# Kernel tuning notes

Hardware: AMD Instinct MI355X
Metric: run time of the kernel (lower is better)

The kernel has to match this reference:

```python
import jax, jax.numpy as jnp
import numpy as np

K = 7      # unfold_size
P = 3      # unfold_size // 2
EPS = 1e-5 # batchnorm eps


def _conv1x1(x, w, b=None):
    # x: (B,C,H,W), w: (O,C)
    y = jnp.einsum('bchw,oc->bohw', x, w)
    if b is not None:
        y = y + b[None, :, None, None]
    return y


def _bn(x, g, b, m, v):
    # eval-mode batchnorm over channel axis 1
    inv = jax.lax.rsqrt(v + EPS)
    return (x - m[None, :, None, None]) * (g * inv)[None, :, None, None] + b[None, :, None, None]


def setup_inputs() -> dict:
    key = jax.random.key(0)
    ks = jax.random.split(key, 18)
    B, C, MID, H, W = 8, 256, 64, 64, 64
    rn = lambda k, s, sc=1.0: jax.random.normal(k, s, dtype=jnp.float32) * sc
    ru = lambda k, s: jax.random.uniform(k, s, dtype=jnp.float32)
    return {
        'x':     rn(ks[0], (B, C, H, W)),
        'w_red': rn(ks[1], (MID, C), 0.05),
        'w_c':   rn(ks[2], (3, MID, MID, 3, 3), 0.05),
        'b_c':   rn(ks[3], (3, MID), 0.05),
        'bn_g':  ru(ks[4], (3, MID)) * 0.5 + 0.75,
        'bn_b':  rn(ks[5], (3, MID), 0.05),
        'bn_m':  rn(ks[6], (3, MID), 0.05),
        'bn_v':  ru(ks[7], (3, MID)) + 0.5,
        'w_out': rn(ks[8], (C, MID), 0.05),
        'b_out': rn(ks[9], (C,), 0.05),
        'bno_g': ru(ks[10], (C,)) * 0.5 + 0.75,
        'bno_b': rn(ks[11], (C,), 0.05),
        'bno_m': rn(ks[12], (C,), 0.05),
        'bno_v': ru(ks[13], (C,)) + 0.5,
        'w_f1':  rn(ks[14], (C, C), 0.05),
        'b_f1':  rn(ks[15], (C,), 0.05),
        'w_f2':  rn(ks[16], (C, C), 0.05),
        'b_f2':  rn(ks[17], (C,), 0.05),
    }


def reference(x, w_red, w_c, b_c, bn_g, bn_b, bn_m, bn_v,
              w_out, b_out, bno_g, bno_b, bno_m, bno_v,
              w_f1, b_f1, w_f2, b_f2):
    B, C, H, W = x.shape
    MID = w_red.shape[0]

    # channel reduction + L2 normalize over channels (F.normalize, eps=1e-12)
    q = _conv1x1(x, w_red)                                   # (B,MID,H,W)
    q = q / jnp.maximum(jnp.linalg.norm(q, axis=1, keepdims=True), 1e-12)

    # SelfCorrelationComputation: unfold KxK with padding P, multiply by center, clamp >= 0
    qp = jnp.pad(q, ((0, 0), (0, 0), (P, P), (P, P)))
    pats = jnp.stack([qp[:, :, i:i + H, j:j + W]
                      for i in range(K) for j in range(K)], axis=2)  # (B,MID,K*K,H,W)
    ss = jnp.maximum(pats * q[:, :, None], 0.0)              # (B,MID,49,H,W)

    # SelfSimilarityEncoder: conv3d with (1,ksize,ksize) kernel == batched 2D conv over (u,v)
    ss = ss.transpose(0, 3, 4, 1, 2).reshape(B * H * W, MID, K, K)  # (B*HW,MID,K,K)
    dn = ('NCHW', 'OIHW', 'NCHW')
    y = ss
    for i in range(3):  # unfold_size // 2 blocks; 7 -> 5 -> 3 -> 1
        y = jax.lax.conv_general_dilated(y, w_c[i], (1, 1), 'VALID', dimension_numbers=dn)
        y = y + b_c[i][None, :, None, None]
        y = jnp.maximum(_bn(y, bn_g[i], bn_b[i], bn_m[i], bn_v[i]), 0.0)
    y = y.mean(axis=(-1, -2)).reshape(B, H, W, MID).transpose(0, 3, 1, 2)  # (B,MID,H,W)
    feat = _bn(_conv1x1(y, w_out, b_out), bno_g, bno_b, bno_m, bno_v)      # (B,C,H,W)

    # residual + FFN (1x1 conv -> relu -> 1x1 conv)
    out = x + feat
    out = _conv1x1(jnp.maximum(_conv1x1(out, w_f1, b_f1), 0.0), w_f2, b_f2)
    return out
```

## Files before the change

kernel.cpp:

```cpp
#include <hip/hip_runtime.h>
#include <stdint.h>


typedef __attribute__((ext_vector_type(8))) __bf16 bf16x8;
typedef __attribute__((ext_vector_type(4))) float f32x4;

__device__ __forceinline__ ushort f2bf(float f) {
  uint32_t u = __builtin_bit_cast(uint32_t, f);
  u += 0x7fffu + ((u >> 16) & 1u);
  return (ushort)(u >> 16);
}
__device__ __forceinline__ float bfu(ushort h) {
  return __builtin_bit_cast(float, ((uint32_t)h) << 16);
}
__device__ __forceinline__ f32x4 mfma16(bf16x8 a, bf16x8 b, f32x4 c) {
  return __builtin_amdgcn_mfma_f32_16x16x32_bf16(a, b, c, 0, 0, 0);
}

union BV8 { uint4 v; ushort u[8]; };

#define OFF_WRT 0u
#define OFF_WCB 65536u
#define OFF_SHC 286720u
#define OFF_WOB 287488u
#define OFF_SHO 320256u
#define OFF_WF1 321280u
#define OFF_WF2 452352u
#define OFF_QN  583424u
#define OFF_Y   4777728u

__global__ __launch_bounds__(256) void k_prep(
    const float* __restrict__ w_red, const float* __restrict__ w_c, const float* __restrict__ b_c,
    const float* __restrict__ bn_g, const float* __restrict__ bn_b, const float* __restrict__ bn_m,
    const float* __restrict__ bn_v, const float* __restrict__ w_out, const float* __restrict__ b_out,
    const float* __restrict__ bno_g, const float* __restrict__ bno_b, const float* __restrict__ bno_m,
    const float* __restrict__ bno_v, const float* __restrict__ w_f1, const float* __restrict__ w_f2,
    float* __restrict__ w_red_t, ushort* __restrict__ wc_b, float* __restrict__ shift_c,
    ushort* __restrict__ w_out_b, float* __restrict__ shift_o,
    ushort* __restrict__ w_f1_b, ushort* __restrict__ w_f2_b)
{
  int i = blockIdx.x * 256 + threadIdx.x;
  if (i < 16384) {
    int c = i >> 6, m = i & 63;
    w_red_t[i] = w_red[m * 256 + c];
    return;
  }
  i -= 16384;
  if (i < 110592) {
    int c = i & 63, o = (i >> 6) & 63, st = i >> 12;
    int tap = st % 9, s = st / 9;
    float sc = bn_g[s * 64 + o] * rsqrtf(bn_v[s * 64 + o] + 1e-5f);
    wc_b[i] = f2bf(w_c[((s * 64 + o) * 64 + c) * 9 + tap] * sc);
    return;
  }
  i -= 110592;
  if (i < 192) {
    int s = i >> 6, o = i & 63;
    float sc = bn_g[s * 64 + o] * rsqrtf(bn_v[s * 64 + o] + 1e-5f);
    shift_c[i] = (b_c[i] - bn_m[i]) * sc + bn_b[i];
    return;
  }
  i -= 192;
  if (i < 16384) {
    int o = i >> 6;
    float sc = bno_g[o] * rsqrtf(bno_v[o] + 1e-5f);
    w_out_b[i] = f2bf(w_out[i] * sc);
    return;
  }
  i -= 16384;
  if (i < 256) {
    float sc = bno_g[i] * rsqrtf(bno_v[i] + 1e-5f);
    shift_o[i] = (b_out[i] - bno_m[i]) * sc + bno_b[i];
    return;
  }
  i -= 256;
  if (i < 65536) { w_f1_b[i] = f2bf(w_f1[i]); return; }
  i -= 65536;
  if (i < 65536) { w_f2_b[i] = f2bf(w_f2[i]); return; }
}

__global__ __launch_bounds__(256) void k_qnorm(
    const float* __restrict__ x, const float* __restrict__ w_red_t, ushort* __restrict__ qn)
{
  __shared__ float xs[64 * 64];
  __shared__ float wls[64 * 64];
  __shared__ float part[64 * 16];
  __shared__ float sinv[64];

  const int tid = threadIdx.x;
  const int pix0 = blockIdx.x * 64;
  const int b = pix0 >> 12;
  const int hw0 = pix0 & 4095;
  const int pxq = tid & 15, mq = tid >> 4;
  const int lr = tid >> 2, lseg = tid & 3;

  float acc[4][4] = {};

  for (int c0 = 0; c0 < 256; c0 += 64) {
    const float4* xg = (const float4*)(x + (size_t)(b * 256 + c0 + lr) * 4096 + hw0 + lseg * 16);
    float4* xd = (float4*)(xs + lr * 64 + lseg * 16);
    const float4* wg = (const float4*)(w_red_t + (c0 + lr) * 64 + lseg * 16);
    float4* wd = (float4*)(wls + lr * 64 + lseg * 16);
#pragma unroll
    for (int j = 0; j < 4; ++j) xd[j] = xg[j];
#pragma unroll
    for (int j = 0; j < 4; ++j) wd[j] = wg[j];
    __syncthreads();
    for (int c = 0; c < 64; ++c) {
      float4 xv = *(const float4*)(xs + c * 64 + pxq * 4);
      float4 wv = *(const float4*)(wls + c * 64 + mq * 4);
      float xa[4] = {xv.x, xv.y, xv.z, xv.w};
      float wa[4] = {wv.x, wv.y, wv.z, wv.w};
#pragma unroll
      for (int mi = 0; mi < 4; ++mi)
#pragma unroll
        for (int pi = 0; pi < 4; ++pi)
          acc[mi][pi] = fmaf(wa[mi], xa[pi], acc[mi][pi]);
    }
    __syncthreads();
  }

#pragma unroll
  for (int pi = 0; pi < 4; ++pi) {
    float s = 0.f;
#pragma unroll
    for (int mi = 0; mi < 4; ++mi) s += acc[mi][pi] * acc[mi][pi];
    part[(pxq * 4 + pi) * 16 + mq] = s;
  }
  __syncthreads();
  if (tid < 64) {
    float s = 0.f;
#pragma unroll
    for (int k = 0; k < 16; ++k) s += part[tid * 16 + k];
    sinv[tid] = 1.0f / fmaxf(sqrtf(s), 1e-12f);
  }
  __syncthreads();
#pragma unroll
  for (int pi = 0; pi < 4; ++pi) {
    const int px = pxq * 4 + pi;
    const float inv = sinv[px];
    ushort4 v;
    v.x = f2bf(acc[0][pi] * inv);
    v.y = f2bf(acc[1][pi] * inv);
    v.z = f2bf(acc[2][pi] * inv);
    v.w = f2bf(acc[3][pi] * inv);
    *(ushort4*)(qn + (size_t)(pix0 + px) * 64 + mq * 4) = v;
  }
}

#define SS_BYTES (49 * 16 * 64 * 2)
#define O1_BYTES (25 * 16 * 64 * 2)
#define SMEM_ENC (SS_BYTES + O1_BYTES)

__device__ __forceinline__ void load_af(bf16x8* af, const ushort* wbase, int o0, int n, int q) {
#pragma unroll
  for (int tap = 0; tap < 9; ++tap)
#pragma unroll
    for (int kc = 0; kc < 2; ++kc)
      af[tap * 2 + kc] = *(const bf16x8*)(wbase + (tap * 64 + o0 + n) * 64 + kc * 32 + q * 8);
}

__device__ __forceinline__ void store_act(ushort* buf, int pos, int n, int q, int o0,
                                          f32x4 acc, float4 sh) {
  ushort4 v;
  v.x = f2bf(fmaxf(acc[0] + sh.x, 0.0f));
  v.y = f2bf(fmaxf(acc[1] + sh.y, 0.0f));
  v.z = f2bf(fmaxf(acc[2] + sh.z, 0.0f));
  v.w = f2bf(fmaxf(acc[3] + sh.w, 0.0f));
  const int chunk = (o0 >> 3) + (q >> 1);
  *(ushort4*)(buf + (pos * 16 + n) * 64 + ((chunk ^ (n & 7)) * 8) + (q & 1) * 4) = v;
}

__global__ __launch_bounds__(512, 1) void k_encoder(
    const ushort* __restrict__ qn, const ushort* __restrict__ wc_b,
    const float* __restrict__ shift_c, ushort* __restrict__ yout)
{
  extern __shared__ char smem[];
  ushort* ss = (ushort*)smem;
  ushort* o1 = (ushort*)(smem + SS_BYTES);
  ushort* o2 = (ushort*)smem;

  const int tid = threadIdx.x;
  const int b = blockIdx.z;
  const int tr = blockIdx.y * 4;
  const int tc = blockIdx.x * 4;

  {
    const int p = tid & 15;
    const int g = tid >> 4;
    const int ph = tr + (p >> 2), pw = tc + (p & 3);
    const ushort* cen = qn + (size_t)((b << 12) + ph * 64 + pw) * 64;
    const int swp = p & 7;
#pragma unroll
    for (int ch = 0; ch < 8; ++ch) {
      BV8 cv; cv.v = *(const uint4*)(cen + ch * 8);
      float cf[8];
#pragma unroll
      for (int j = 0; j < 8; ++j) cf[j] = bfu(cv.u[j]);
      for (int uv = g; uv < 49; uv += 32) {
        const int du = uv / 7 - 3, dv = uv % 7 - 3;
        const int nh = ph + du, nw = pw + dv;
        BV8 ov;
        if ((unsigned)nh < 64u && (unsigned)nw < 64u) {
          BV8 nv; nv.v = *(const uint4*)(qn + (size_t)((b << 12) + nh * 64 + nw) * 64 + ch * 8);
#pragma unroll
          for (int j = 0; j < 8; ++j)
            ov.u[j] = f2bf(fmaxf(bfu(nv.u[j]) * cf[j], 0.0f));
        } else {
          ov.v = make_uint4(0u, 0u, 0u, 0u);
        }
        *(uint4*)(ss + (uv * 16 + p) * 64 + ((ch ^ swp) * 8)) = ov.v;
      }
    }
  }
  __syncthreads();

  const int lane = tid & 63, wv = tid >> 6;
  const int n = lane & 15, q = lane >> 4;
  const int o0 = (wv & 3) * 16;
  const int h = wv >> 2;
  const int sw = n & 7;
  const int rowoff = n * 64;
  const int c0 = ((0 + q) ^ sw) * 8;
  const int c1 = ((4 + q) ^ sw) * 8;

  bf16x8 af[18];
  const f32x4 zero = {0.f, 0.f, 0.f, 0.f};

  load_af(af, wc_b, o0, n, q);
  {
    const float4 sh = *(const float4*)(shift_c + o0 + q * 4);
    const int ubeg = h ? 3 : 0, uend = h ? 5 : 3;
    for (int u = ubeg; u < uend; ++u) {
      f32x4 acc[5][2];
#pragma unroll
      for (int v = 0; v < 5; ++v) { acc[v][0] = zero; acc[v][1] = zero; }
#pragma unroll
      for (int du = 0; du < 3; ++du) {
        const ushort* rowb = ss + (u + du) * 7 * 1024 + rowoff;
        bf16x8 rf0[7], rf1[7];
#pragma unroll
        for (int j = 0; j < 7; ++j) {
          rf0[j] = *(const bf16x8*)(rowb + j * 1024 + c0);
          rf1[j] = *(const bf16x8*)(rowb + j * 1024 + c1);
        }
#pragma unroll
        for (int dv = 0; dv < 3; ++dv) {
#pragma unroll
          for (int v = 0; v < 5; ++v) {
            acc[v][0] = mfma16(af[(du * 3 + dv) * 2],     rf0[v + dv], acc[v][0]);
            acc[v][1] = mfma16(af[(du * 3 + dv) * 2 + 1], rf1[v + dv], acc[v][1]);
          }
        }
      }
#pragma unroll
      for (int v = 0; v < 5; ++v)
        store_act(o1, u * 5 + v, n, q, o0, acc[v][0] + acc[v][1], sh);
    }
  }
  __syncthreads();

  load_af(af, wc_b + 9 * 4096, o0, n, q);
  {
    const float4 sh = *(const float4*)(shift_c + 64 + o0 + q * 4);
    const int ubeg = h ? 2 : 0, uend = h ? 3 : 2;
    for (int u = ubeg; u < uend; ++u) {
      f32x4 acc[3][2];
#pragma unroll
      for (int v = 0; v < 3; ++v) { acc[v][0] = zero; acc[v][1] = zero; }
#pragma unroll
      for (int du = 0; du < 3; ++du) {
        const ushort* rowb = o1 + (u + du) * 5 * 1024 + rowoff;
        bf16x8 rf0[5], rf1[5];
#pragma unroll
        for (int j = 0; j < 5; ++j) {
          rf0[j] = *(const bf16x8*)(rowb + j * 1024 + c0);
          rf1[j] = *(const bf16x8*)(rowb + j * 1024 + c1);
        }
#pragma unroll
        for (int dv = 0; dv < 3; ++dv) {
#pragma unroll
          for (int v = 0; v < 3; ++v) {
            acc[v][0] = mfma16(af[(du * 3 + dv) * 2],     rf0[v + dv], acc[v][0]);
            acc[v][1] = mfma16(af[(du * 3 + dv) * 2 + 1], rf1[v + dv], acc[v][1]);
          }
        }
      }
#pragma unroll
      for (int v = 0; v < 3; ++v)
        store_act(o2, u * 3 + v, n, q, o0, acc[v][0] + acc[v][1], sh);
    }
  }
  __syncthreads();

  if (h == 0) {
    load_af(af, wc_b + 18 * 4096, o0, n, q);
    const float4 sh = *(const float4*)(shift_c + 128 + o0 + q * 4);
    f32x4 a0 = zero, a1 = zero;
#pragma unroll
    for (int tap = 0; tap < 9; ++tap) {
      const ushort* rA = o2 + tap * 1024 + rowoff;
      a0 = mfma16(af[tap * 2],     *(const bf16x8*)(rA + c0), a0);
      a1 = mfma16(af[tap * 2 + 1], *(const bf16x8*)(rA + c1), a1);
    }
    f32x4 acc = a0 + a1;
    ushort4 v;
    v.x = f2bf(fmaxf(acc[0] + sh.x, 0.0f));
    v.y = f2bf(fmaxf(acc[1] + sh.y, 0.0f));
    v.z = f2bf(fmaxf(acc[2] + sh.z, 0.0f));
    v.w = f2bf(fmaxf(acc[3] + sh.w, 0.0f));
    const int ph = tr + (n >> 2), pw = tc + (n & 3);
    *(ushort4*)(yout + (size_t)((b << 12) + ph * 64 + pw) * 64 + o0 + q * 4) = v;
  }
}

#define SMEM_OUT (2 * 64 * 256 * 2)

__global__ __launch_bounds__(256) void k_out(
    const ushort* __restrict__ y, const float* __restrict__ x,
    const ushort* __restrict__ w_out_b, const float* __restrict__ shift_o,
    const ushort* __restrict__ w_f1_b, const float* __restrict__ b_f1,
    const ushort* __restrict__ w_f2_b, const float* __restrict__ b_f2,
    float* __restrict__ out)
{
  extern __shared__ char smem[];
  ushort* rls = (ushort*)smem;
  ushort* hls = (ushort*)(smem + 64 * 256 * 2);

  const int tid = threadIdx.x, lane = tid & 63, wv = tid >> 6;
  const int n = lane & 15, q = lane >> 4;
  const int pix0 = blockIdx.x * 64;
  const int b = pix0 >> 12, hw0 = pix0 & 4095;
  const int sw = n & 7;
  const f32x4 zero = {0.f, 0.f, 0.f, 0.f};

  {
    bf16x8 wa[8];
#pragma unroll
    for (int mt = 0; mt < 4; ++mt) {
      const int ob = wv * 64 + mt * 16;
      wa[mt * 2]     = *(const bf16x8*)(w_out_b + (ob + n) * 64 + q * 8);
      wa[mt * 2 + 1] = *(const bf16x8*)(w_out_b + (ob + n) * 64 + 32 + q * 8);
    }
    for (int nt = 0; nt < 4; ++nt) {
      const int px0 = nt * 16;
      const bf16x8 yb0 = *(const bf16x8*)(y + (size_t)(pix0 + px0 + n) * 64 + q * 8);
      const bf16x8 yb1 = *(const bf16x8*)(y + (size_t)(pix0 + px0 + n) * 64 + 32 + q * 8);
#pragma unroll
      for (int mt = 0; mt < 4; ++mt) {
        const int ob = wv * 64 + mt * 16;
        f32x4 acc = zero;
        acc = mfma16(wa[mt * 2], yb0, acc);
        acc = mfma16(wa[mt * 2 + 1], yb1, acc);
        const float4 sh = *(const float4*)(shift_o + ob + q * 4);
        const float sha[4] = {sh.x, sh.y, sh.z, sh.w};
        ushort tmp[4];
#pragma unroll
        for (int r = 0; r < 4; ++r) {
          const int o = ob + q * 4 + r;
          const float xv = x[(size_t)(b * 256 + o) * 4096 + hw0 + px0 + n];
          tmp[r] = f2bf(xv + acc[r] + sha[r]);
        }
        ushort4 v; v.x = tmp[0]; v.y = tmp[1]; v.z = tmp[2]; v.w = tmp[3];
        const int chunk = (ob >> 3) + (q >> 1);
        *(ushort4*)(rls + (px0 + n) * 256 + ((chunk ^ sw) * 8) + (q & 1) * 4) = v;
      }
    }
  }
  __syncthreads();

  {
    bf16x8 wf[32];
#pragma unroll
    for (int mt = 0; mt < 4; ++mt)
#pragma unroll
      for (int kc = 0; kc < 8; ++kc)
        wf[mt * 8 + kc] = *(const bf16x8*)(w_f1_b + (size_t)(wv * 64 + mt * 16 + n) * 256 + kc * 32 + q * 8);
    for (int nt = 0; nt < 4; ++nt) {
      const int px0 = nt * 16;
      bf16x8 rb[8];
#pragma unroll
      for (int kc = 0; kc < 8; ++kc)
        rb[kc] = *(const bf16x8*)(rls + (px0 + n) * 256 + (((kc * 4 + q) ^ sw) * 8));
#pragma unroll
      for (int mt = 0; mt < 4; ++mt) {
        const int ob = wv * 64 + mt * 16;
        f32x4 a0 = zero, a1 = zero;
#pragma unroll
        for (int kc = 0; kc < 8; kc += 2) {
          a0 = mfma16(wf[mt * 8 + kc], rb[kc], a0);
          a1 = mfma16(wf[mt * 8 + kc + 1], rb[kc + 1], a1);
        }
        f32x4 acc = a0 + a1;
        const float4 bb = *(const float4*)(b_f1 + ob + q * 4);
        const float bba[4] = {bb.x, bb.y, bb.z, bb.w};
        ushort tmp[4];
#pragma unroll
        for (int r = 0; r < 4; ++r) tmp[r] = f2bf(fmaxf(acc[r] + bba[r], 0.0f));
        ushort4 v; v.x = tmp[0]; v.y = tmp[1]; v.z = tmp[2]; v.w = tmp[3];
        const int chunk = (ob >> 3) + (q >> 1);
        *(ushort4*)(hls + (px0 + n) * 256 + ((chunk ^ sw) * 8) + (q & 1) * 4) = v;
      }
    }
  }
  __syncthreads();

  {
    bf16x8 wf[32];
#pragma unroll
    for (int mt = 0; mt < 4; ++mt)
#pragma unroll
      for (int kc = 0; kc < 8; ++kc)
        wf[mt * 8 + kc] = *(const bf16x8*)(w_f2_b + (size_t)(wv * 64 + mt * 16 + n) * 256 + kc * 32 + q * 8);
    for (int nt = 0; nt < 4; ++nt) {
      const int px0 = nt * 16;
      bf16x8 rb[8];
#pragma unroll
      for (int kc = 0; kc < 8; ++kc)
        rb[kc] = *(const bf16x8*)(hls + (px0 + n) * 256 + (((kc * 4 + q) ^ sw) * 8));
#pragma unroll
      for (int mt = 0; mt < 4; ++mt) {
        const int ob = wv * 64 + mt * 16;
        f32x4 a0 = zero, a1 = zero;
#pragma unroll
        for (int kc = 0; kc < 8; kc += 2) {
          a0 = mfma16(wf[mt * 8 + kc], rb[kc], a0);
          a1 = mfma16(wf[mt * 8 + kc + 1], rb[kc + 1], a1);
        }
        f32x4 acc = a0 + a1;
        const float4 bb = *(const float4*)(b_f2 + ob + q * 4);
        const float bba[4] = {bb.x, bb.y, bb.z, bb.w};
#pragma unroll
        for (int r = 0; r < 4; ++r) {
          const int o = ob + q * 4 + r;
          out[(size_t)(b * 256 + o) * 4096 + hw0 + px0 + n] = acc[r] + bba[r];
        }
      }
    }
  }
}

extern "C" void kernel_launch(void* const* d_in, const int* in_sizes, int n_in,
                              void* d_out, int out_size, void* d_ws, size_t ws_size,
                              hipStream_t stream) {
  const float* x     = (const float*)d_in[0];
  const float* w_red = (const float*)d_in[1];
  const float* w_c   = (const float*)d_in[2];
  const float* b_c   = (const float*)d_in[3];
  const float* bn_g  = (const float*)d_in[4];
  const float* bn_b  = (const float*)d_in[5];
  const float* bn_m  = (const float*)d_in[6];
  const float* bn_v  = (const float*)d_in[7];
  const float* w_out = (const float*)d_in[8];
  const float* b_out = (const float*)d_in[9];
  const float* bno_g = (const float*)d_in[10];
  const float* bno_b = (const float*)d_in[11];
  const float* bno_m = (const float*)d_in[12];
  const float* bno_v = (const float*)d_in[13];
  const float* w_f1  = (const float*)d_in[14];
  const float* b_f1  = (const float*)d_in[15];
  const float* w_f2  = (const float*)d_in[16];
  const float* b_f2  = (const float*)d_in[17];

  char* ws = (char*)d_ws;
  float*  w_red_t = (float*)(ws + OFF_WRT);
  ushort* wc_b    = (ushort*)(ws + OFF_WCB);
  float*  shift_c = (float*)(ws + OFF_SHC);
  ushort* w_out_b = (ushort*)(ws + OFF_WOB);
  float*  shift_o = (float*)(ws + OFF_SHO);
  ushort* w_f1_b  = (ushort*)(ws + OFF_WF1);
  ushort* w_f2_b  = (ushort*)(ws + OFF_WF2);
  ushort* qnb     = (ushort*)(ws + OFF_QN);
  ushort* yb      = (ushort*)(ws + OFF_Y);

  k_prep<<<1074, 256, 0, stream>>>(w_red, w_c, b_c, bn_g, bn_b, bn_m, bn_v,
                                   w_out, b_out, bno_g, bno_b, bno_m, bno_v,
                                   w_f1, w_f2,
                                   w_red_t, wc_b, shift_c, w_out_b, shift_o, w_f1_b, w_f2_b);
  k_qnorm<<<512, 256, 0, stream>>>(x, w_red_t, qnb);
  k_encoder<<<dim3(16, 16, 8), 512, SMEM_ENC, stream>>>(qnb, wc_b, shift_c, yb);
  k_out<<<512, 256, SMEM_OUT, stream>>>(yb, x, w_out_b, shift_o, w_f1_b, b_f1, w_f2_b, b_f2,
                                        (float*)d_out);
}
```

Measured before the change: 323.7 us.

## Double encoder block to 1024 threads with templated 4-way conv work split

The encoder block now launches 1024 threads (16 waves) instead of 512. Each conv stage's output positions are split four ways across wave groups through a templated conv_block, and the K dimension is walked in two sequential halves so each wave holds only 9 weight fragments instead of 18. The self-similarity build gives each thread one fixed neighbor offset instead of a strided loop. The aim is more waves for latency hiding and lower register pressure, at the cost of an unbalanced split in the last stage and reloading weights per half.

```diff
diff --git a/kernel.cpp b/kernel.cpp
--- a/kernel.cpp
+++ b/kernel.cpp
@@ -152,14 +152,6 @@
 #define O1_BYTES (25 * 16 * 64 * 2)
 #define SMEM_ENC (SS_BYTES + O1_BYTES)
 
-__device__ __forceinline__ void load_af(bf16x8* af, const ushort* wbase, int o0, int n, int q) {
-#pragma unroll
-  for (int tap = 0; tap < 9; ++tap)
-#pragma unroll
-    for (int kc = 0; kc < 2; ++kc)
-      af[tap * 2 + kc] = *(const bf16x8*)(wbase + (tap * 64 + o0 + n) * 64 + kc * 32 + q * 8);
-}
-
 __device__ __forceinline__ void store_act(ushort* buf, int pos, int n, int q, int o0,
                                           f32x4 acc, float4 sh) {
   ushort4 v;
@@ -171,7 +163,53 @@
   *(ushort4*)(buf + (pos * 16 + n) * 64 + ((chunk ^ (n & 7)) * 8) + (q & 1) * 4) = v;
 }
 
-__global__ __launch_bounds__(512, 1) void k_encoder(
+template<int RS, int DS, int UB, int UE, int VB, int VE>
+__device__ __forceinline__ void conv_block(
+    const ushort* __restrict__ src, ushort* dst,
+    const ushort* __restrict__ wbase, const float* __restrict__ shiftp,
+    int n, int q, int o0, int rowoff, int c0, int c1)
+{
+  constexpr int NU = UE - UB, NV = VE - VB, NR = VE + 2 - VB;
+  const f32x4 zero = {0.f, 0.f, 0.f, 0.f};
+  f32x4 acc[NU][NV];
+#pragma unroll
+  for (int a = 0; a < NU; ++a)
+#pragma unroll
+    for (int bb = 0; bb < NV; ++bb) acc[a][bb] = zero;
+
+#pragma unroll 1
+  for (int kc = 0; kc < 2; ++kc) {
+    const int cc = kc ? c1 : c0;
+    bf16x8 af[9];
+#pragma unroll
+    for (int t = 0; t < 9; ++t)
+      af[t] = *(const bf16x8*)(wbase + (t * 64 + o0 + n) * 64 + kc * 32 + q * 8);
+#pragma unroll
+    for (int u = UB; u < UE; ++u) {
+#pragma unroll
+      for (int du = 0; du < 3; ++du) {
+        const ushort* rowb = src + (u + du) * RS * 1024 + rowoff;
+        bf16x8 rf[NR];
+#pragma unroll
+        for (int j = 0; j < NR; ++j)
+          rf[j] = *(const bf16x8*)(rowb + (VB + j) * 1024 + cc);
+#pragma unroll
+        for (int dv = 0; dv < 3; ++dv)
+#pragma unroll
+          for (int v = 0; v < NV; ++v)
+            acc[u - UB][v] = mfma16(af[du * 3 + dv], rf[v + dv], acc[u - UB][v]);
+      }
+    }
+  }
+  const float4 sh = *(const float4*)(shiftp + o0 + q * 4);
+#pragma unroll
+  for (int u = UB; u < UE; ++u)
+#pragma unroll
+    for (int v = 0; v < NV; ++v)
+      store_act(dst, u * DS + VB + v, n, q, o0, acc[u - UB][v], sh);
+}
+
+__global__ __launch_bounds__(1024) void k_encoder(
     const ushort* __restrict__ qn, const ushort* __restrict__ wc_b,
     const float* __restrict__ shift_c, ushort* __restrict__ yout)
 {
@@ -188,28 +226,29 @@
   {
     const int p = tid & 15;
     const int g = tid >> 4;
-    const int ph = tr + (p >> 2), pw = tc + (p & 3);
-    const ushort* cen = qn + (size_t)((b << 12) + ph * 64 + pw) * 64;
-    const int swp = p & 7;
-#pragma unroll
-    for (int ch = 0; ch < 8; ++ch) {
-      BV8 cv; cv.v = *(const uint4*)(cen + ch * 8);
-      float cf[8];
-#pragma unroll
-      for (int j = 0; j < 8; ++j) cf[j] = bfu(cv.u[j]);
-      for (int uv = g; uv < 49; uv += 32) {
-        const int du = uv / 7 - 3, dv = uv % 7 - 3;
-        const int nh = ph + du, nw = pw + dv;
-        BV8 ov;
-        if ((unsigned)nh < 64u && (unsigned)nw < 64u) {
-          BV8 nv; nv.v = *(const uint4*)(qn + (size_t)((b << 12) + nh * 64 + nw) * 64 + ch * 8);
+    if (g < 49) {
+      const int ph = tr + (p >> 2), pw = tc + (p & 3);
+      const ushort* cen = qn + (size_t)((b << 12) + ph * 64 + pw) * 64;
+      const int swp = p & 7;
+      const int du = g / 7 - 3, dv = g % 7 - 3;
+      const int nh = ph + du, nw = pw + dv;
+      if ((unsigned)nh < 64u && (unsigned)nw < 64u) {
+        const ushort* nb = qn + (size_t)((b << 12) + nh * 64 + nw) * 64;
+#pragma unroll
+        for (int ch = 0; ch < 8; ++ch) {
+          BV8 cv; cv.v = *(const uint4*)(cen + ch * 8);
+          BV8 nv; nv.v = *(const uint4*)(nb + ch * 8);
+          BV8 ov;
 #pragma unroll
           for (int j = 0; j < 8; ++j)
-            ov.u[j] = f2bf(fmaxf(bfu(nv.u[j]) * cf[j], 0.0f));
-        } else {
-          ov.v = make_uint4(0u, 0u, 0u, 0u);
+            ov.u[j] = f2bf(fmaxf(bfu(nv.u[j]) * bfu(cv.u[j]), 0.0f));
+          *(uint4*)(ss + (g * 16 + p) * 64 + ((ch ^ swp) * 8)) = ov.v;
         }
-        *(uint4*)(ss + (uv * 16 + p) * 64 + ((ch ^ swp) * 8)) = ov.v;
+      } else {
+        const uint4 z = make_uint4(0u, 0u, 0u, 0u);
+#pragma unroll
+        for (int ch = 0; ch < 8; ++ch)
+          *(uint4*)(ss + (g * 16 + p) * 64 + ((ch ^ swp) * 8)) = z;
       }
     }
   }
@@ -218,92 +257,54 @@
   const int lane = tid & 63, wv = tid >> 6;
   const int n = lane & 15, q = lane >> 4;
   const int o0 = (wv & 3) * 16;
-  const int h = wv >> 2;
+  const int G = wv >> 2;
   const int sw = n & 7;
   const int rowoff = n * 64;
   const int c0 = ((0 + q) ^ sw) * 8;
   const int c1 = ((4 + q) ^ sw) * 8;
 
-  bf16x8 af[18];
-  const f32x4 zero = {0.f, 0.f, 0.f, 0.f};
-
-  load_af(af, wc_b, o0, n, q);
-  {
-    const float4 sh = *(const float4*)(shift_c + o0 + q * 4);
-    const int ubeg = h ? 3 : 0, uend = h ? 5 : 3;
-    for (int u = ubeg; u < uend; ++u) {
-      f32x4 acc[5][2];
-#pragma unroll
-      for (int v = 0; v < 5; ++v) { acc[v][0] = zero; acc[v][1] = zero; }
-#pragma unroll
-      for (int du = 0; du < 3; ++du) {
-        const ushort* rowb = ss + (u + du) * 7 * 1024 + rowoff;
-        bf16x8 rf0[7], rf1[7];
-#pragma unroll
-        for (int j = 0; j < 7; ++j) {
-          rf0[j] = *(const bf16x8*)(rowb + j * 1024 + c0);
-          rf1[j] = *(const bf16x8*)(rowb + j * 1024 + c1);
-        }
-#pragma unroll
-        for (int dv = 0; dv < 3; ++dv) {
-#pragma unroll
-          for (int v = 0; v < 5; ++v) {
-            acc[v][0] = mfma16(af[(du * 3 + dv) * 2],     rf0[v + dv], acc[v][0]);
-            acc[v][1] = mfma16(af[(du * 3 + dv) * 2 + 1], rf1[v + dv], acc[v][1]);
-          }
-        }
-      }
-#pragma unroll
-      for (int v = 0; v < 5; ++v)
-        store_act(o1, u * 5 + v, n, q, o0, acc[v][0] + acc[v][1], sh);
-    }
-  }
-  __syncthreads();
-
-  load_af(af, wc_b + 9 * 4096, o0, n, q);
-  {
-    const float4 sh = *(const float4*)(shift_c + 64 + o0 + q * 4);
-    const int ubeg = h ? 2 : 0, uend = h ? 3 : 2;
-    for (int u = ubeg; u < uend; ++u) {
-      f32x4 acc[3][2];
-#pragma unroll
-      for (int v = 0; v < 3; ++v) { acc[v][0] = zero; acc[v][1] = zero; }
-#pragma unroll
-      for (int du = 0; du < 3; ++du) {
-        const ushort* rowb = o1 + (u + du) * 5 * 1024 + rowoff;
-        bf16x8 rf0[5], rf1[5];
-#pragma unroll
-        for (int j = 0; j < 5; ++j) {
-          rf0[j] = *(const bf16x8*)(rowb + j * 1024 + c0);
-          rf1[j] = *(const bf16x8*)(rowb + j * 1024 + c1);
-        }
-#pragma unroll
-        for (int dv = 0; dv < 3; ++dv) {
-#pragma unroll
-          for (int v = 0; v < 3; ++v) {
-            acc[v][0] = mfma16(af[(du * 3 + dv) * 2],     rf0[v + dv], acc[v][0]);
-            acc[v][1] = mfma16(af[(du * 3 + dv) * 2 + 1], rf1[v + dv], acc[v][1]);
-          }
-        }
-      }
-#pragma unroll
-      for (int v = 0; v < 3; ++v)
-        store_act(o2, u * 3 + v, n, q, o0, acc[v][0] + acc[v][1], sh);
-    }
-  }
-  __syncthreads();
-
-  if (h == 0) {
-    load_af(af, wc_b + 18 * 4096, o0, n, q);
+  {
+    const ushort* w1 = wc_b;
+    if (G == 0)
+      conv_block<7, 5, 0, 2, 0, 5>(ss, o1, w1, shift_c, n, q, o0, rowoff, c0, c1);
+    else if (G == 1)
+      conv_block<7, 5, 2, 4, 0, 5>(ss, o1, w1, shift_c, n, q, o0, rowoff, c0, c1);
+    else if (G == 2)
+      conv_block<7, 5, 4, 5, 0, 3>(ss, o1, w1, shift_c, n, q, o0, rowoff, c0, c1);
+    else
+      conv_block<7, 5, 4, 5, 3, 5>(ss, o1, w1, shift_c, n, q, o0, rowoff, c0, c1);
+  }
+  __syncthreads();
+
+  {
+    const ushort* w2 = wc_b + 9 * 4096;
+    const float* sh2 = shift_c + 64;
+    if (G == 0)
+      conv_block<5, 3, 0, 1, 0, 3>(o1, o2, w2, sh2, n, q, o0, rowoff, c0, c1);
+    else if (G == 1)
+      conv_block<5, 3, 1, 2, 0, 3>(o1, o2, w2, sh2, n, q, o0, rowoff, c0, c1);
+    else if (G == 2)
+      conv_block<5, 3, 2, 3, 0, 2>(o1, o2, w2, sh2, n, q, o0, rowoff, c0, c1);
+    else
+      conv_block<5, 3, 2, 3, 2, 3>(o1, o2, w2, sh2, n, q, o0, rowoff, c0, c1);
+  }
+  __syncthreads();
+
+  if (G == 0) {
+    const ushort* w3 = wc_b + 18 * 4096;
+    const f32x4 zero = {0.f, 0.f, 0.f, 0.f};
+    f32x4 acc = zero;
+#pragma unroll 1
+    for (int kc = 0; kc < 2; ++kc) {
+      const int cc = kc ? c1 : c0;
+#pragma unroll
+      for (int t = 0; t < 9; ++t) {
+        bf16x8 a = *(const bf16x8*)(w3 + (t * 64 + o0 + n) * 64 + kc * 32 + q * 8);
+        bf16x8 r = *(const bf16x8*)(o2 + t * 1024 + rowoff + cc);
+        acc = mfma16(a, r, acc);
+      }
+    }
     const float4 sh = *(const float4*)(shift_c + 128 + o0 + q * 4);
-    f32x4 a0 = zero, a1 = zero;
-#pragma unroll
-    for (int tap = 0; tap < 9; ++tap) {
-      const ushort* rA = o2 + tap * 1024 + rowoff;
-      a0 = mfma16(af[tap * 2],     *(const bf16x8*)(rA + c0), a0);
-      a1 = mfma16(af[tap * 2 + 1], *(const bf16x8*)(rA + c1), a1);
-    }
-    f32x4 acc = a0 + a1;
     ushort4 v;
     v.x = f2bf(fmaxf(acc[0] + sh.x, 0.0f));
     v.y = f2bf(fmaxf(acc[1] + sh.y, 0.0f));
@@ -478,7 +479,7 @@
                                    w_f1, w_f2,
                                    w_red_t, wc_b, shift_c, w_out_b, shift_o, w_f1_b, w_f2_b);
   k_qnorm<<<512, 256, 0, stream>>>(x, w_red_t, qnb);
-  k_encoder<<<dim3(16, 16, 8), 512, SMEM_ENC, stream>>>(qnb, wc_b, shift_c, yb);
+  k_encoder<<<dim3(16, 16, 8), 1024, SMEM_ENC, stream>>>(qnb, wc_b, shift_c, yb);
   k_out<<<512, 256, SMEM_OUT, stream>>>(yb, x, w_out_b, shift_o, w_f1_b, b_f1, w_f2_b, b_f2,
                                         (float*)d_out);
 }
```

Measured after the change: 366.8 us. 13.3% more time.

## Restructure encoder convs to load each input row once and raise occupancy

Applied to the files above, without the earlier changes.

Replaces the per-output-row conv loops with a templated conv2d_block that walks input rows once and accumulates into all output rows that use each row, cutting redundant LDS reads of shared rows. Each output position now uses a single accumulator chain instead of two split halves. Launch bounds are changed to allow two blocks per CU. The aim is fewer LDS loads and more latency hiding, at the cost of more live accumulator registers, which may cause spills or keep occupancy from rising given the large shared memory footprint.

```diff
diff --git a/kernel.cpp b/kernel.cpp
--- a/kernel.cpp
+++ b/kernel.cpp
@@ -152,14 +152,6 @@
 #define O1_BYTES (25 * 16 * 64 * 2)
 #define SMEM_ENC (SS_BYTES + O1_BYTES)
 
-__device__ __forceinline__ void load_af(bf16x8* af, const ushort* wbase, int o0, int n, int q) {
-#pragma unroll
-  for (int tap = 0; tap < 9; ++tap)
-#pragma unroll
-    for (int kc = 0; kc < 2; ++kc)
-      af[tap * 2 + kc] = *(const bf16x8*)(wbase + (tap * 64 + o0 + n) * 64 + kc * 32 + q * 8);
-}
-
 __device__ __forceinline__ void store_act(ushort* buf, int pos, int n, int q, int o0,
                                           f32x4 acc, float4 sh) {
   ushort4 v;
@@ -171,7 +163,59 @@
   *(ushort4*)(buf + (pos * 16 + n) * 64 + ((chunk ^ (n & 7)) * 8) + (q & 1) * 4) = v;
 }
 
-__global__ __launch_bounds__(512, 1) void k_encoder(
+template<int RS, int OS, int UB, int UE>
+__device__ __forceinline__ void conv2d_block(
+    const ushort* __restrict__ src, ushort* dst,
+    const ushort* __restrict__ wbase, const float* __restrict__ shiftp,
+    int n, int q, int o0, int rowoff, int c0, int c1)
+{
+  constexpr int NU = UE - UB, NV = OS, NP = OS + 2;
+  const f32x4 zero = {0.f, 0.f, 0.f, 0.f};
+  f32x4 acc[NU][NV];
+#pragma unroll
+  for (int a = 0; a < NU; ++a)
+#pragma unroll
+    for (int bb = 0; bb < NV; ++bb) acc[a][bb] = zero;
+
+  bf16x8 af[18];
+#pragma unroll
+  for (int t = 0; t < 9; ++t) {
+    af[t * 2]     = *(const bf16x8*)(wbase + (t * 64 + o0 + n) * 64 + q * 8);
+    af[t * 2 + 1] = *(const bf16x8*)(wbase + (t * 64 + o0 + n) * 64 + 32 + q * 8);
+  }
+
+#pragma unroll
+  for (int ir = UB; ir < UE + 2; ++ir) {
+    const ushort* rowb = src + ir * RS * 1024 + rowoff;
+    bf16x8 rf0[NP], rf1[NP];
+#pragma unroll
+    for (int j = 0; j < NP; ++j) {
+      rf0[j] = *(const bf16x8*)(rowb + j * 1024 + c0);
+      rf1[j] = *(const bf16x8*)(rowb + j * 1024 + c1);
+    }
+#pragma unroll
+    for (int u = UB; u < UE; ++u) {
+      if (ir - u >= 0 && ir - u < 3) {
+        const int du = ir - u;
+#pragma unroll
+        for (int dv = 0; dv < 3; ++dv)
+#pragma unroll
+          for (int v = 0; v < NV; ++v) {
+            acc[u - UB][v] = mfma16(af[(du * 3 + dv) * 2],     rf0[v + dv], acc[u - UB][v]);
+            acc[u - UB][v] = mfma16(af[(du * 3 + dv) * 2 + 1], rf1[v + dv], acc[u - UB][v]);
+          }
+      }
+    }
+  }
+  const float4 sh = *(const float4*)(shiftp + o0 + q * 4);
+#pragma unroll
+  for (int u = 0; u < NU; ++u)
+#pragma unroll
+    for (int v = 0; v < NV; ++v)
+      store_act(dst, (UB + u) * OS + v, n, q, o0, acc[u][v], sh);
+}
+
+__global__ __launch_bounds__(512, 2) void k_encoder(
     const ushort* __restrict__ qn, const ushort* __restrict__ wc_b,
     const float* __restrict__ shift_c, ushort* __restrict__ yout)
 {
@@ -224,86 +268,32 @@
   const int c0 = ((0 + q) ^ sw) * 8;
   const int c1 = ((4 + q) ^ sw) * 8;
 
-  bf16x8 af[18];
-  const f32x4 zero = {0.f, 0.f, 0.f, 0.f};
-
-  load_af(af, wc_b, o0, n, q);
-  {
-    const float4 sh = *(const float4*)(shift_c + o0 + q * 4);
-    const int ubeg = h ? 3 : 0, uend = h ? 5 : 3;
-    for (int u = ubeg; u < uend; ++u) {
-      f32x4 acc[5][2];
-#pragma unroll
-      for (int v = 0; v < 5; ++v) { acc[v][0] = zero; acc[v][1] = zero; }
-#pragma unroll
-      for (int du = 0; du < 3; ++du) {
-        const ushort* rowb = ss + (u + du) * 7 * 1024 + rowoff;
-        bf16x8 rf0[7], rf1[7];
-#pragma unroll
-        for (int j = 0; j < 7; ++j) {
-          rf0[j] = *(const bf16x8*)(rowb + j * 1024 + c0);
-          rf1[j] = *(const bf16x8*)(rowb + j * 1024 + c1);
-        }
-#pragma unroll
-        for (int dv = 0; dv < 3; ++dv) {
-#pragma unroll
-          for (int v = 0; v < 5; ++v) {
-            acc[v][0] = mfma16(af[(du * 3 + dv) * 2],     rf0[v + dv], acc[v][0]);
-            acc[v][1] = mfma16(af[(du * 3 + dv) * 2 + 1], rf1[v + dv], acc[v][1]);
-          }
-        }
-      }
-#pragma unroll
-      for (int v = 0; v < 5; ++v)
-        store_act(o1, u * 5 + v, n, q, o0, acc[v][0] + acc[v][1], sh);
-    }
-  }
-  __syncthreads();
-
-  load_af(af, wc_b + 9 * 4096, o0, n, q);
-  {
-    const float4 sh = *(const float4*)(shift_c + 64 + o0 + q * 4);
-    const int ubeg = h ? 2 : 0, uend = h ? 3 : 2;
-    for (int u = ubeg; u < uend; ++u) {
-      f32x4 acc[3][2];
-#pragma unroll
-      for (int v = 0; v < 3; ++v) { acc[v][0] = zero; acc[v][1] = zero; }
-#pragma unroll
-      for (int du = 0; du < 3; ++du) {
-        const ushort* rowb = o1 + (u + du) * 5 * 1024 + rowoff;
-        bf16x8 rf0[5], rf1[5];
-#pragma unroll
-        for (int j = 0; j < 5; ++j) {
-          rf0[j] = *(const bf16x8*)(rowb + j * 1024 + c0);
-          rf1[j] = *(const bf16x8*)(rowb + j * 1024 + c1);
-        }
-#pragma unroll
-        for (int dv = 0; dv < 3; ++dv) {
-#pragma unroll
-          for (int v = 0; v < 3; ++v) {
-            acc[v][0] = mfma16(af[(du * 3 + dv) * 2],     rf0[v + dv], acc[v][0]);
-            acc[v][1] = mfma16(af[(du * 3 + dv) * 2 + 1], rf1[v + dv], acc[v][1]);
-          }
-        }
-      }
-#pragma unroll
-      for (int v = 0; v < 3; ++v)
-        store_act(o2, u * 3 + v, n, q, o0, acc[v][0] + acc[v][1], sh);
-    }
-  }
+  if (h == 0)
+    conv2d_block<7, 5, 0, 3>(ss, o1, wc_b, shift_c, n, q, o0, rowoff, c0, c1);
+  else
+    conv2d_block<7, 5, 3, 5>(ss, o1, wc_b, shift_c, n, q, o0, rowoff, c0, c1);
+  __syncthreads();
+
+  if (h == 0)
+    conv2d_block<5, 3, 0, 2>(o1, o2, wc_b + 9 * 4096, shift_c + 64, n, q, o0, rowoff, c0, c1);
+  else
+    conv2d_block<5, 3, 2, 3>(o1, o2, wc_b + 9 * 4096, shift_c + 64, n, q, o0, rowoff, c0, c1);
   __syncthreads();
 
   if (h == 0) {
-    load_af(af, wc_b + 18 * 4096, o0, n, q);
+    const ushort* w3 = wc_b + 18 * 4096;
+    const f32x4 zero = {0.f, 0.f, 0.f, 0.f};
+    f32x4 a0 = zero, a1 = zero;
+#pragma unroll
+    for (int tap = 0; tap < 9; ++tap) {
+      bf16x8 wf0 = *(const bf16x8*)(w3 + (tap * 64 + o0 + n) * 64 + q * 8);
+      bf16x8 wf1 = *(const bf16x8*)(w3 + (tap * 64 + o0 + n) * 64 + 32 + q * 8);
+      const ushort* rA = o2 + tap * 1024 + rowoff;
+      a0 = mfma16(wf0, *(const bf16x8*)(rA + c0), a0);
+      a1 = mfma16(wf1, *(const bf16x8*)(rA + c1), a1);
+    }
+    f32x4 acc = a0 + a1;
     const float4 sh = *(const float4*)(shift_c + 128 + o0 + q * 4);
-    f32x4 a0 = zero, a1 = zero;
-#pragma unroll
-    for (int tap = 0; tap < 9; ++tap) {
-      const ushort* rA = o2 + tap * 1024 + rowoff;
-      a0 = mfma16(af[tap * 2],     *(const bf16x8*)(rA + c0), a0);
-      a1 = mfma16(af[tap * 2 + 1], *(const bf16x8*)(rA + c1), a1);
-    }
-    f32x4 acc = a0 + a1;
     ushort4 v;
     v.x = f2bf(fmaxf(acc[0] + sh.x, 0.0f));
     v.y = f2bf(fmaxf(acc[1] + sh.y, 0.0f));
```

After: 321.4 us. Within noise of the previous version (-0.7%).

## Stream encoder self-similarity rows through double-buffered LDS ring with 256-thread blocks

Applied to the files above, without the earlier changes.

The encoder no longer materializes all 49 self-similarity taps in LDS before the first conv. It builds one unfold row at a time into a two-slot ring, overlaps building the next row with MFMA work on the current row, and accumulates all 25 first-layer outputs in registers. The block is shrunk to 256 threads (4 waves, one per 16-channel slice) with launch bounds allowing 2 blocks per CU, and LDS per block is cut so two blocks can co-reside. The cost is more accumulator registers (25 f32x4 per lane) and therefore spill risk, plus each wave now doing all rows of the second conv instead of splitting them.

```diff
diff --git a/kernel.cpp b/kernel.cpp
--- a/kernel.cpp
+++ b/kernel.cpp
@@ -148,17 +148,9 @@
   }
 }
 
-#define SS_BYTES (49 * 16 * 64 * 2)
-#define O1_BYTES (25 * 16 * 64 * 2)
-#define SMEM_ENC (SS_BYTES + O1_BYTES)
-
-__device__ __forceinline__ void load_af(bf16x8* af, const ushort* wbase, int o0, int n, int q) {
-#pragma unroll
-  for (int tap = 0; tap < 9; ++tap)
-#pragma unroll
-    for (int kc = 0; kc < 2; ++kc)
-      af[tap * 2 + kc] = *(const bf16x8*)(wbase + (tap * 64 + o0 + n) * 64 + kc * 32 + q * 8);
-}
+#define ENC_RING 7168
+#define ENC_O1   14336
+#define SMEM_ENC 79872
 
 __device__ __forceinline__ void store_act(ushort* buf, int pos, int n, int q, int o0,
                                           f32x4 acc, float4 sh) {
@@ -171,144 +163,171 @@
   *(ushort4*)(buf + (pos * 16 + n) * 64 + ((chunk ^ (n & 7)) * 8) + (q & 1) * 4) = v;
 }
 
-__global__ __launch_bounds__(512, 1) void k_encoder(
+__device__ __forceinline__ void build_row(
+    ushort* dstslot, const ushort* __restrict__ qn,
+    int b, int tr, int tc, int ir, int tid)
+{
+  for (int u0 = tid; u0 < 896; u0 += 256) {
+    const int ch = u0 & 7, px = (u0 >> 3) & 15, dv = u0 >> 7;
+    const int ph = tr + (px >> 2), pw = tc + (px & 3);
+    const int nh = ph + ir - 3, nw = pw + dv - 3;
+    uint4 ov4;
+    if ((unsigned)nh < 64u && (unsigned)nw < 64u) {
+      BV8 cv; cv.v = *(const uint4*)(qn + (size_t)((b << 12) + ph * 64 + pw) * 64 + ch * 8);
+      BV8 nv; nv.v = *(const uint4*)(qn + (size_t)((b << 12) + nh * 64 + nw) * 64 + ch * 8);
+      BV8 ov;
+#pragma unroll
+      for (int j = 0; j < 8; ++j)
+        ov.u[j] = f2bf(fmaxf(bfu(nv.u[j]) * bfu(cv.u[j]), 0.0f));
+      ov4 = ov.v;
+    } else {
+      ov4 = make_uint4(0u, 0u, 0u, 0u);
+    }
+    *(uint4*)(dstslot + (dv * 16 + px) * 64 + ((ch ^ (px & 7)) * 8)) = ov4;
+  }
+}
+
+__global__ __launch_bounds__(256, 2) void k_encoder(
     const ushort* __restrict__ qn, const ushort* __restrict__ wc_b,
     const float* __restrict__ shift_c, ushort* __restrict__ yout)
 {
   extern __shared__ char smem[];
-  ushort* ss = (ushort*)smem;
-  ushort* o1 = (ushort*)(smem + SS_BYTES);
-  ushort* o2 = (ushort*)smem;
+  ushort* enc = (ushort*)smem;
+  ushort* o1 = enc + ENC_O1;
 
   const int tid = threadIdx.x;
   const int b = blockIdx.z;
   const int tr = blockIdx.y * 4;
   const int tc = blockIdx.x * 4;
 
-  {
-    const int p = tid & 15;
-    const int g = tid >> 4;
-    const int ph = tr + (p >> 2), pw = tc + (p & 3);
-    const ushort* cen = qn + (size_t)((b << 12) + ph * 64 + pw) * 64;
-    const int swp = p & 7;
-#pragma unroll
-    for (int ch = 0; ch < 8; ++ch) {
-      BV8 cv; cv.v = *(const uint4*)(cen + ch * 8);
-      float cf[8];
-#pragma unroll
-      for (int j = 0; j < 8; ++j) cf[j] = bfu(cv.u[j]);
-      for (int uv = g; uv < 49; uv += 32) {
-        const int du = uv / 7 - 3, dv = uv % 7 - 3;
-        const int nh = ph + du, nw = pw + dv;
-        BV8 ov;
-        if ((unsigned)nh < 64u && (unsigned)nw < 64u) {
-          BV8 nv; nv.v = *(const uint4*)(qn + (size_t)((b << 12) + nh * 64 + nw) * 64 + ch * 8);
-#pragma unroll
-          for (int j = 0; j < 8; ++j)
-            ov.u[j] = f2bf(fmaxf(bfu(nv.u[j]) * cf[j], 0.0f));
-        } else {
-          ov.v = make_uint4(0u, 0u, 0u, 0u);
-        }
-        *(uint4*)(ss + (uv * 16 + p) * 64 + ((ch ^ swp) * 8)) = ov.v;
-      }
-    }
-  }
-  __syncthreads();
-
   const int lane = tid & 63, wv = tid >> 6;
   const int n = lane & 15, q = lane >> 4;
-  const int o0 = (wv & 3) * 16;
-  const int h = wv >> 2;
+  const int o0 = wv * 16;
   const int sw = n & 7;
   const int rowoff = n * 64;
   const int c0 = ((0 + q) ^ sw) * 8;
   const int c1 = ((4 + q) ^ sw) * 8;
 
   bf16x8 af[18];
+#pragma unroll
+  for (int t = 0; t < 9; ++t) {
+    af[t * 2]     = *(const bf16x8*)(wc_b + (t * 64 + o0 + n) * 64 + q * 8);
+    af[t * 2 + 1] = *(const bf16x8*)(wc_b + (t * 64 + o0 + n) * 64 + 32 + q * 8);
+  }
+
   const f32x4 zero = {0.f, 0.f, 0.f, 0.f};
-
-  load_af(af, wc_b, o0, n, q);
+  f32x4 acc[5][5];
+#pragma unroll
+  for (int u = 0; u < 5; ++u)
+#pragma unroll
+    for (int v = 0; v < 5; ++v) acc[u][v] = zero;
+
+  build_row(enc, qn, b, tr, tc, 0, tid);
+  __syncthreads();
+
+#pragma unroll
+  for (int ir = 0; ir < 7; ++ir) {
+    if (ir < 6)
+      build_row(enc + ((ir + 1) & 1) * ENC_RING, qn, b, tr, tc, ir + 1, tid);
+    {
+      const ushort* rowb = enc + (ir & 1) * ENC_RING + rowoff;
+      bf16x8 rf0[7], rf1[7];
+#pragma unroll
+      for (int j = 0; j < 7; ++j) {
+        rf0[j] = *(const bf16x8*)(rowb + j * 1024 + c0);
+        rf1[j] = *(const bf16x8*)(rowb + j * 1024 + c1);
+      }
+#pragma unroll
+      for (int u = 0; u < 5; ++u) {
+        const int du = ir - u;
+        if (du >= 0 && du < 3) {
+#pragma unroll
+          for (int dv = 0; dv < 3; ++dv)
+#pragma unroll
+            for (int v = 0; v < 5; ++v) {
+              acc[u][v] = mfma16(af[(du * 3 + dv) * 2],     rf0[v + dv], acc[u][v]);
+              acc[u][v] = mfma16(af[(du * 3 + dv) * 2 + 1], rf1[v + dv], acc[u][v]);
+            }
+        }
+      }
+    }
+    if (ir < 6) __syncthreads();
+  }
+
   {
     const float4 sh = *(const float4*)(shift_c + o0 + q * 4);
-    const int ubeg = h ? 3 : 0, uend = h ? 5 : 3;
-    for (int u = ubeg; u < uend; ++u) {
-      f32x4 acc[5][2];
-#pragma unroll
-      for (int v = 0; v < 5; ++v) { acc[v][0] = zero; acc[v][1] = zero; }
-#pragma unroll
-      for (int du = 0; du < 3; ++du) {
-        const ushort* rowb = ss + (u + du) * 7 * 1024 + rowoff;
-        bf16x8 rf0[7], rf1[7];
-#pragma unroll
-        for (int j = 0; j < 7; ++j) {
-          rf0[j] = *(const bf16x8*)(rowb + j * 1024 + c0);
-          rf1[j] = *(const bf16x8*)(rowb + j * 1024 + c1);
+#pragma unroll
+    for (int u = 0; u < 5; ++u)
+#pragma unroll
+      for (int v = 0; v < 5; ++v)
+        store_act(o1, u * 5 + v, n, q, o0, acc[u][v], sh);
+  }
+  __syncthreads();
+
+  {
+#pragma unroll
+    for (int t = 0; t < 9; ++t) {
+      af[t * 2]     = *(const bf16x8*)(wc_b + 9 * 4096 + (t * 64 + o0 + n) * 64 + q * 8);
+      af[t * 2 + 1] = *(const bf16x8*)(wc_b + 9 * 4096 + (t * 64 + o0 + n) * 64 + 32 + q * 8);
+    }
+    f32x4 acc2[3][3];
+#pragma unroll
+    for (int u = 0; u < 3; ++u)
+#pragma unroll
+      for (int v = 0; v < 3; ++v) acc2[u][v] = zero;
+
+#pragma unroll
+    for (int ir = 0; ir < 5; ++ir) {
+      const ushort* rowb = o1 + ir * 5 * 1024 + rowoff;
+      bf16x8 rf0[5], rf1[5];
+#pragma unroll
+      for (int j = 0; j < 5; ++j) {
+        rf0[j] = *(const bf16x8*)(rowb + j * 1024 + c0);
+        rf1[j] = *(const bf16x8*)(rowb + j * 1024 + c1);
+      }
+#pragma unroll
+      for (int u = 0; u < 3; ++u) {
+        const int du = ir - u;
+        if (du >= 0 && du < 3) {
+#pragma unroll
+          for (int dv = 0; dv < 3; ++dv)
+#pragma unroll
+            for (int v = 0; v < 3; ++v) {
+              acc2[u][v] = mfma16(af[(du * 3 + dv) * 2],     rf0[v + dv], acc2[u][v]);
+              acc2[u][v] = mfma16(af[(du * 3 + dv) * 2 + 1], rf1[v + dv], acc2[u][v]);
+            }
         }
-#pragma unroll
-        for (int dv = 0; dv < 3; ++dv) {
-#pragma unroll
-          for (int v = 0; v < 5; ++v) {
-            acc[v][0] = mfma16(af[(du * 3 + dv) * 2],     rf0[v + dv], acc[v][0]);
-            acc[v][1] = mfma16(af[(du * 3 + dv) * 2 + 1], rf1[v + dv], acc[v][1]);
-          }
-        }
-      }
-#pragma unroll
-      for (int v = 0; v < 5; ++v)
-        store_act(o1, u * 5 + v, n, q, o0, acc[v][0] + acc[v][1], sh);
-    }
-  }
-  __syncthreads();
-
-  load_af(af, wc_b + 9 * 4096, o0, n, q);
+      }
+    }
+    const float4 sh = *(const float4*)(shift_c + 64 + o0 + q * 4);
+#pragma unroll
+    for (int u = 0; u < 3; ++u)
+#pragma unroll
+      for (int v = 0; v < 3; ++v)
+        store_act(enc, u * 3 + v, n, q, o0, acc2[u][v], sh);
+  }
+  __syncthreads();
+
   {
-    const float4 sh = *(const float4*)(shift_c + 64 + o0 + q * 4);
-    const int ubeg = h ? 2 : 0, uend = h ? 3 : 2;
-    for (int u = ubeg; u < uend; ++u) {
-      f32x4 acc[3][2];
-#pragma unroll
-      for (int v = 0; v < 3; ++v) { acc[v][0] = zero; acc[v][1] = zero; }
-#pragma unroll
-      for (int du = 0; du < 3; ++du) {
-        const ushort* rowb = o1 + (u + du) * 5 * 1024 + rowoff;
-        bf16x8 rf0[5], rf1[5];
-#pragma unroll
-        for (int j = 0; j < 5; ++j) {
-          rf0[j] = *(const bf16x8*)(rowb + j * 1024 + c0);
-          rf1[j] = *(const bf16x8*)(rowb + j * 1024 + c1);
-        }
-#pragma unroll
-        for (int dv = 0; dv < 3; ++dv) {
-#pragma unroll
-          for (int v = 0; v < 3; ++v) {
-            acc[v][0] = mfma16(af[(du * 3 + dv) * 2],     rf0[v + dv], acc[v][0]);
-            acc[v][1] = mfma16(af[(du * 3 + dv) * 2 + 1], rf1[v + dv], acc[v][1]);
-          }
-        }
-      }
-#pragma unroll
-      for (int v = 0; v < 3; ++v)
-        store_act(o2, u * 3 + v, n, q, o0, acc[v][0] + acc[v][1], sh);
-    }
-  }
-  __syncthreads();
-
-  if (h == 0) {
-    load_af(af, wc_b + 18 * 4096, o0, n, q);
-    const float4 sh = *(const float4*)(shift_c + 128 + o0 + q * 4);
+#pragma unroll
+    for (int t = 0; t < 9; ++t) {
+      af[t * 2]     = *(const bf16x8*)(wc_b + 18 * 4096 + (t * 64 + o0 + n) * 64 + q * 8);
+      af[t * 2 + 1] = *(const bf16x8*)(wc_b + 18 * 4096 + (t * 64 + o0 + n) * 64 + 32 + q * 8);
+    }
     f32x4 a0 = zero, a1 = zero;
 #pragma unroll
     for (int tap = 0; tap < 9; ++tap) {
-      const ushort* rA = o2 + tap * 1024 + rowoff;
+      const ushort* rA = enc + tap * 1024 + rowoff;
       a0 = mfma16(af[tap * 2],     *(const bf16x8*)(rA + c0), a0);
       a1 = mfma16(af[tap * 2 + 1], *(const bf16x8*)(rA + c1), a1);
     }
-    f32x4 acc = a0 + a1;
+    f32x4 acc3 = a0 + a1;
+    const float4 sh = *(const float4*)(shift_c + 128 + o0 + q * 4);
     ushort4 v;
-    v.x = f2bf(fmaxf(acc[0] + sh.x, 0.0f));
-    v.y = f2bf(fmaxf(acc[1] + sh.y, 0.0f));
-    v.z = f2bf(fmaxf(acc[2] + sh.z, 0.0f));
-    v.w = f2bf(fmaxf(acc[3] + sh.w, 0.0f));
+    v.x = f2bf(fmaxf(acc3[0] + sh.x, 0.0f));
+    v.y = f2bf(fmaxf(acc3[1] + sh.y, 0.0f));
+    v.z = f2bf(fmaxf(acc3[2] + sh.z, 0.0f));
+    v.w = f2bf(fmaxf(acc3[3] + sh.w, 0.0f));
     const int ph = tr + (n >> 2), pw = tc + (n & 3);
     *(ushort4*)(yout + (size_t)((b << 12) + ph * 64 + pw) * 64 + o0 + q * 4) = v;
   }
@@ -478,7 +497,7 @@
                                    w_f1, w_f2,
                                    w_red_t, wc_b, shift_c, w_out_b, shift_o, w_f1_b, w_f2_b);
   k_qnorm<<<512, 256, 0, stream>>>(x, w_red_t, qnb);
-  k_encoder<<<dim3(16, 16, 8), 512, SMEM_ENC, stream>>>(qnb, wc_b, shift_c, yb);
+  k_encoder<<<dim3(16, 16, 8), 256, SMEM_ENC, stream>>>(qnb, wc_b, shift_c, yb);
   k_out<<<512, 256, SMEM_OUT, stream>>>(yb, x, w_out_b, shift_o, w_f1_b, b_f1, w_f2_b, b_f2,
                                         (float*)d_out);
 }
```

After: 273.6 us. 15.5% less time.
